# Kernel tuning notes

Hardware: AMD Instinct MI355X
Metric: run time of the kernel (lower is better)

## Reference

```python
import jax, jax.numpy as jnp
import numpy as np

N, E = 50000, 800000
IN, HID, OUT, H = 128, 16, 16, 4


def setup_inputs() -> dict:
    key = jax.random.key(0)
    ks = jax.random.split(key, 11)
    sc = 0.1
    return {
        "features": jax.random.normal(ks[0], (N, IN), jnp.float32),
        "src": jax.random.randint(ks[1], (E,), 0, N, dtype=jnp.int64) if jax.config.jax_enable_x64 else jax.random.randint(ks[1], (E,), 0, N).astype(jnp.int32),
        "dst": jax.random.randint(ks[2], (E,), 0, N).astype(jnp.int32),
        "W1": jax.random.normal(ks[3], (H * HID, IN), jnp.float32) * sc,
        "al1": jax.random.normal(ks[4], (H, HID), jnp.float32) * sc,
        "ar1": jax.random.normal(ks[5], (H, HID), jnp.float32) * sc,
        "b1": jax.random.normal(ks[6], (H * HID,), jnp.float32) * sc,
        "W2": jax.random.normal(ks[7], (H * OUT, H * HID), jnp.float32) * sc,
        "al2": jax.random.normal(ks[8], (H, OUT), jnp.float32) * sc,
        "ar2": jax.random.normal(ks[9], (H, OUT), jnp.float32) * sc,
        "b2": jax.random.normal(ks[10], (H * OUT,), jnp.float32) * sc,
    }


def gat_conv(src, dst, feat, W, al, ar, b, heads, dout):
    """DGL-style GATConv: fc -> edge attention -> dst-softmax -> scatter-sum."""
    n = feat.shape[0]
    h = (feat @ W.T).reshape(n, heads, dout)            # [N,H,D]
    el = jnp.einsum("nhd,hd->nh", h, al)                # [N,H]
    er = jnp.einsum("nhd,hd->nh", h, ar)                # [N,H]
    e = jax.nn.leaky_relu(el[src] + er[dst], 0.2)       # [E,H]
    m = jax.ops.segment_max(e, dst, num_segments=n)     # per-dst max, [N,H]
    a = jnp.exp(e - m[dst])                             # [E,H]
    s = jax.ops.segment_sum(a, dst, num_segments=n)     # [N,H]
    alpha = a / s[dst]                                  # edge softmax, [E,H]
    out = jax.ops.segment_sum(alpha[:, :, None] * h[src], dst, num_segments=n)
    return out + b.reshape(1, heads, dout)              # [N,H,D]


def reference(features, src, dst, W1, al1, ar1, b1, W2, al2, ar2, b2):
    h = gat_conv(src, dst, features, W1, al1, ar1, b1, H, HID).reshape(N, H * HID)
    h = jax.nn.relu(h)
    h = gat_conv(src, dst, h, W2, al2, ar2, b2, H, OUT).mean(axis=1)  # mean over heads
    return jax.nn.log_softmax(h, axis=1)
```

## Files before the change

### kernel.cpp

```cpp
#include <hip/hip_runtime.h>
#include <math.h>

#define N_NODES 50000
#define N_EDGES 800000
#define NPART 8
#define PART_SZ ((N_NODES + NPART - 1) / NPART)
#define CAP 64
#define SCAT_BLOCKS 2048

typedef __attribute__((ext_vector_type(8))) short short8;
typedef __attribute__((ext_vector_type(8))) unsigned short ushort8;
typedef __attribute__((ext_vector_type(4))) float v4f;
typedef __attribute__((ext_vector_type(2))) float v2f;
typedef __attribute__((ext_vector_type(4))) int int4v;

__device__ __forceinline__ float bf2f(unsigned short h) {
    return __uint_as_float(((unsigned int)h) << 16);
}
__device__ __forceinline__ unsigned short f2bf(float f) {
    unsigned int u = __float_as_uint(f);
    u += 0x7fff + ((u >> 16) & 1);
    return (unsigned short)(u >> 16);
}

__device__ __forceinline__ short8 load_afrag(const float* X, size_t row, int K,
                                             int kc, int quad) {
    const float* p = X + row * K + kc * 32 + quad * 8;
    const float4 t0 = *(const float4*)p;
    const float4 t1 = *(const float4*)(p + 4);
    short8 a;
    a[0] = (short)f2bf(t0.x); a[1] = (short)f2bf(t0.y);
    a[2] = (short)f2bf(t0.z); a[3] = (short)f2bf(t0.w);
    a[4] = (short)f2bf(t1.x); a[5] = (short)f2bf(t1.y);
    a[6] = (short)f2bf(t1.z); a[7] = (short)f2bf(t1.w);
    return a;
}
__device__ __forceinline__ short8 load_afrag(const unsigned short* X, size_t row,
                                             int K, int kc, int quad) {
    return *(const short8*)(X + row * K + kc * 32 + quad * 8);
}

template <int K, typename XT>
__global__ __launch_bounds__(256) void fc_att_mfma(
    const XT* __restrict__ X, const float* __restrict__ W,
    const float* __restrict__ al, const float* __restrict__ ar,
    unsigned short* __restrict__ Hout, float* __restrict__ el,
    float* __restrict__ er, int nTiles)
{
    constexpr int KP = K + 4;
    constexpr int NKC = K / 32;
    __shared__ float Wlds[64 * KP];
    const int tid = threadIdx.x;
    for (int i = tid; i < 64 * K; i += 256) {
        int r = i / K, c = i - r * K;
        Wlds[r * KP + c] = W[i];
    }
    __syncthreads();

    const int lane = tid & 63;
    const int wave = tid >> 6;
    const int d = lane & 15;
    const int quad = lane >> 4;

    short8 wf[4][NKC];
#pragma unroll
    for (int ng = 0; ng < 4; ++ng) {
#pragma unroll
        for (int kc = 0; kc < NKC; ++kc) {
            const float* wp = &Wlds[(ng * 16 + d) * KP + kc * 32 + quad * 8];
            const v4f w0 = *(const v4f*)wp;
            const v4f w1 = *(const v4f*)(wp + 4);
            short8 f;
            f[0] = (short)f2bf(w0[0]); f[1] = (short)f2bf(w0[1]);
            f[2] = (short)f2bf(w0[2]); f[3] = (short)f2bf(w0[3]);
            f[4] = (short)f2bf(w1[0]); f[5] = (short)f2bf(w1[1]);
            f[6] = (short)f2bf(w1[2]); f[7] = (short)f2bf(w1[3]);
            wf[ng][kc] = f;
        }
    }

    const int tile = blockIdx.x * 4 + wave;
    if (tile >= nTiles) return;
    const int node0 = tile * 16;

    v4f cc[4] = {{0.f,0.f,0.f,0.f},{0.f,0.f,0.f,0.f},{0.f,0.f,0.f,0.f},{0.f,0.f,0.f,0.f}};
#pragma unroll
    for (int kc = 0; kc < NKC; ++kc) {
        const short8 a = load_afrag(X, (size_t)(node0 + d), K, kc, quad);
        cc[0] = __builtin_amdgcn_mfma_f32_16x16x32_bf16(a, wf[0][kc], cc[0], 0, 0, 0);
        cc[1] = __builtin_amdgcn_mfma_f32_16x16x32_bf16(a, wf[1][kc], cc[1], 0, 0, 0);
        cc[2] = __builtin_amdgcn_mfma_f32_16x16x32_bf16(a, wf[2][kc], cc[2], 0, 0, 0);
        cc[3] = __builtin_amdgcn_mfma_f32_16x16x32_bf16(a, wf[3][kc], cc[3], 0, 0, 0);
    }

#pragma unroll
    for (int ng = 0; ng < 4; ++ng) {
        const float alv = al[ng * 16 + d];
        const float arv = ar[ng * 16 + d];
        const v4f c = cc[ng];
#pragma unroll
        for (int r = 0; r < 4; ++r) {
            const int node = node0 + quad * 4 + r;
            Hout[(size_t)node * 64 + ng * 16 + d] = f2bf(c[r]);
            float vel = c[r] * alv;
            float ver = c[r] * arv;
#pragma unroll
            for (int off = 1; off < 16; off <<= 1) {
                vel += __shfl_xor(vel, off);
                ver += __shfl_xor(ver, off);
            }
            if (d == 0) {
                el[node * 4 + ng] = vel;
                er[node * 4 + ng] = ver;
            }
        }
    }
}

__device__ __forceinline__ void scat1(int d, int s, int lo, int hi,
                                      int* __restrict__ cnt16,
                                      unsigned short* __restrict__ col)
{
    if (d >= lo && d < hi) {
        const int pos = atomicAdd(&cnt16[(unsigned)d * 16], 1);
        if (pos < CAP) col[(unsigned)d * CAP + pos] = (unsigned short)s;
    }
}

__global__ __launch_bounds__(256) void scatter_bucket_kernel(
    const int* __restrict__ src, const int* __restrict__ dst,
    int* __restrict__ cnt16, unsigned short* __restrict__ col)
{
    const int part = blockIdx.x & (NPART - 1);
    const int lo = part * PART_SZ;
    const int hi = lo + PART_SZ;
    const int tid_p = ((int)blockIdx.x >> 3) * 256 + threadIdx.x;
    const int stride = (SCAT_BLOCKS / NPART) * 256;
    const int4v* dst4 = (const int4v*)dst;
    const int4v* src4 = (const int4v*)src;
    const int NQ = N_EDGES / 4;
    for (int q = tid_p; q < NQ; q += 2 * stride) {
        const int q2 = q + stride;
        const bool ok2 = q2 < NQ;
        const int4v dA = __builtin_nontemporal_load(dst4 + q);
        const int4v sA = __builtin_nontemporal_load(src4 + q);
        const int4v dB = ok2 ? __builtin_nontemporal_load(dst4 + q2) : (int4v){-1,-1,-1,-1};
        const int4v sB = ok2 ? __builtin_nontemporal_load(src4 + q2) : (int4v){0,0,0,0};
        scat1(dA[0], sA[0], lo, hi, cnt16, col);
        scat1(dA[1], sA[1], lo, hi, cnt16, col);
        scat1(dA[2], sA[2], lo, hi, cnt16, col);
        scat1(dA[3], sA[3], lo, hi, cnt16, col);
        scat1(dB[0], sB[0], lo, hi, cnt16, col);
        scat1(dB[1], sB[1], lo, hi, cnt16, col);
        scat1(dB[2], sB[2], lo, hi, cnt16, col);
        scat1(dB[3], sB[3], lo, hi, cnt16, col);
    }
}

__device__ __forceinline__ void agg_walk_pair(
    const unsigned short* __restrict__ colrow, int len, int len_max,
    const float* __restrict__ el, const unsigned int* __restrict__ Hf32,
    int hb, int hl, float erv_a,
    float& accL_out, float& accH_out, float& sacc_a_out)
{
    const int j_a = hl >> 2;
    const unsigned h_a = (unsigned)(hl & 3);
    const int hd = hl >> 3;
    float accL0 = 0.f, accL1 = 0.f, accH0 = 0.f, accH1 = 0.f;
    float sacc_a = 0.f;
    for (int i = 0; i < len_max; i += 16) {
        const ushort8 sv0 = __builtin_nontemporal_load((const ushort8*)(colrow + i));
        const ushort8 sv1 = __builtin_nontemporal_load((const ushort8*)(colrow + i + 8));
        const int rm = len - i;
        const unsigned sa0 = (unsigned)colrow[i + j_a];
        const unsigned sa1 = (unsigned)colrow[i + 8 + j_a];
        float x0 = el[sa0 * 4u + h_a] + erv_a;
        float x1 = el[sa1 * 4u + h_a] + erv_a;
        x0 = fmaxf(x0, 0.2f * x0);
        x1 = fmaxf(x1, 0.2f * x1);
        float a0 = __expf(x0);
        float a1 = __expf(x1);
        a0 = (j_a < rm) ? a0 : 0.f;
        a1 = (j_a + 8 < rm) ? a1 : 0.f;
        sacc_a += a0 + a1;
        unsigned uu[16];
#pragma unroll
        for (int j = 0; j < 8; ++j)
            uu[j] = Hf32[(unsigned)sv0[j] * 32u + (unsigned)hl];
#pragma unroll
        for (int j = 0; j < 8; ++j)
            uu[8 + j] = Hf32[(unsigned)sv1[j] * 32u + (unsigned)hl];
#pragma unroll
        for (int j = 0; j < 8; ++j) {
            const float aj = __shfl(a0, hb + j * 4 + hd);
            const float lo = __uint_as_float(uu[j] << 16);
            const float hi = __uint_as_float(uu[j] & 0xffff0000u);
            if (j & 1) { accL1 = fmaf(aj, lo, accL1); accH1 = fmaf(aj, hi, accH1); }
            else       { accL0 = fmaf(aj, lo, accL0); accH0 = fmaf(aj, hi, accH0); }
        }
#pragma unroll
        for (int j = 0; j < 8; ++j) {
            const float aj = __shfl(a1, hb + j * 4 + hd);
            const float lo = __uint_as_float(uu[8 + j] << 16);
            const float hi = __uint_as_float(uu[8 + j] & 0xffff0000u);
            if (j & 1) { accL1 = fmaf(aj, lo, accL1); accH1 = fmaf(aj, hi, accH1); }
            else       { accL0 = fmaf(aj, lo, accL0); accH0 = fmaf(aj, hi, accH0); }
        }
    }
    sacc_a += __shfl_xor(sacc_a, 4);
    sacc_a += __shfl_xor(sacc_a, 8);
    sacc_a += __shfl_xor(sacc_a, 16);
    sacc_a_out = sacc_a;
    accL_out = accL0 + accL1;
    accH_out = accH0 + accH1;
}

__global__ __launch_bounds__(256) void agg_relu_kernel(
    const int* __restrict__ cnt16, const unsigned short* __restrict__ col,
    const float* __restrict__ el, const float* __restrict__ er,
    const unsigned int* __restrict__ Hf32, const float* __restrict__ b,
    unsigned int* __restrict__ out32, int n)
{
    const int lane = threadIdx.x & 63;
    const int wave = threadIdx.x >> 6;
    const int hl = lane & 31;
    const int hb = lane & 32;
    const int node = blockIdx.x * 8 + wave * 2 + (lane >> 5);
    if (node >= n) return;
    const int hd = hl >> 3;
    const int cg = hd * 16 + (hl & 7) * 2;
    const float erv_a = er[node * 4 + (hl & 3)];
    const int len = min(cnt16[(unsigned)node * 16], CAP);
    const int len_max = max(len, __shfl_xor(len, 32));
    float accL, accH, sacc_a;
    agg_walk_pair(col + (unsigned)node * CAP, len, len_max, el, Hf32,
                  hb, hl, erv_a, accL, accH, sacc_a);
    const float sc = __shfl(sacc_a, hb + hd);
    float vL = sc > 0.f ? accL / sc : 0.f;
    float vH = sc > 0.f ? accH / sc : 0.f;
    vL += b[cg];   vH += b[cg + 1];
    vL = vL > 0.f ? vL : 0.f;
    vH = vH > 0.f ? vH : 0.f;
    const unsigned u = (unsigned)f2bf(vL) | ((unsigned)f2bf(vH) << 16);
    __builtin_nontemporal_store(u, out32 + (size_t)node * 32 + hl);
}

__global__ __launch_bounds__(256) void agg_final_kernel(
    const int* __restrict__ cnt16, const unsigned short* __restrict__ col,
    const float* __restrict__ el, const float* __restrict__ er,
    const unsigned int* __restrict__ Hf32, const float* __restrict__ b,
    float* __restrict__ out, int n)
{
    const int lane = threadIdx.x & 63;
    const int wave = threadIdx.x >> 6;
    const int hl = lane & 31;
    const int hb = lane & 32;
    const int node = blockIdx.x * 8 + wave * 2 + (lane >> 5);
    if (node >= n) return;
    const int hd = hl >> 3;
    const int cg = hd * 16 + (hl & 7) * 2;
    const float erv_a = er[node * 4 + (hl & 3)];
    const int len = min(cnt16[(unsigned)node * 16], CAP);
    const int len_max = max(len, __shfl_xor(len, 32));
    float accL, accH, sacc_a;
    agg_walk_pair(col + (unsigned)node * CAP, len, len_max, el, Hf32,
                  hb, hl, erv_a, accL, accH, sacc_a);
    const float sc = __shfl(sacc_a, hb + hd);
    float zL = sc > 0.f ? accL / sc : 0.f;
    float zH = sc > 0.f ? accH / sc : 0.f;
    zL += b[cg];   zH += b[cg + 1];
    zL += __shfl_xor(zL, 8);  zL += __shfl_xor(zL, 16);  zL *= 0.25f;
    zH += __shfl_xor(zH, 8);  zH += __shfl_xor(zH, 16);  zH *= 0.25f;
    float m = fmaxf(zL, zH);
    m = fmaxf(m, __shfl_xor(m, 1));
    m = fmaxf(m, __shfl_xor(m, 2));
    m = fmaxf(m, __shfl_xor(m, 4));
    float se = __expf(zL - m) + __expf(zH - m);
    se += __shfl_xor(se, 1);
    se += __shfl_xor(se, 2);
    se += __shfl_xor(se, 4);
    const float lse = __logf(se);
    if (hl < 8) {
        v2f r;
        r[0] = zL - m - lse;
        r[1] = zH - m - lse;
        __builtin_nontemporal_store(r, (v2f*)(out + (size_t)node * 16 + hl * 2));
    }
}

extern "C" void kernel_launch(void* const* d_in, const int* in_sizes, int n_in,
                              void* d_out, int out_size, void* d_ws, size_t ws_size,
                              hipStream_t stream)
{
    const float* feat = (const float*)d_in[0];
    const int*   src  = (const int*)d_in[1];
    const int*   dst  = (const int*)d_in[2];
    const float* W1   = (const float*)d_in[3];
    const float* al1  = (const float*)d_in[4];
    const float* ar1  = (const float*)d_in[5];
    const float* b1   = (const float*)d_in[6];
    const float* W2   = (const float*)d_in[7];
    const float* al2  = (const float*)d_in[8];
    const float* ar2  = (const float*)d_in[9];
    const float* b2   = (const float*)d_in[10];
    float* out = (float*)d_out;

    float* el  = (float*)d_ws;
    float* er  = el + N_NODES * 4;
    int*   cnt16 = (int*)(er + N_NODES * 4);
    uintptr_t p = ((uintptr_t)(cnt16 + N_NODES * 16) + 15) & ~(uintptr_t)15;
    unsigned short* col = (unsigned short*)p;
    unsigned short* A   = col + (size_t)N_NODES * CAP + 64;
    unsigned short* B   = A + (size_t)N_NODES * 64;

    const int NT = N_NODES / 16;
    const int FB = (NT + 3) / 4;
    const int AB2 = (N_NODES + 7) / 8;

    (void)hipMemsetAsync(cnt16, 0, (size_t)((char*)A - (char*)cnt16), stream);
    scatter_bucket_kernel<<<SCAT_BLOCKS, 256, 0, stream>>>(src, dst, cnt16, col);

    fc_att_mfma<128, float><<<FB, 256, 0, stream>>>(feat, W1, al1, ar1, A, el, er, NT);
    agg_relu_kernel<<<AB2, 256, 0, stream>>>(cnt16, col, el, er,
                                             (const unsigned int*)A, b1,
                                             (unsigned int*)B, N_NODES);

    fc_att_mfma<64, unsigned short><<<FB, 256, 0, stream>>>(B, W2, al2, ar2, A, el, er, NT);
    agg_final_kernel<<<AB2, 256, 0, stream>>>(cnt16, col, el, er,
                                              (const unsigned int*)A, b2, out, N_NODES);
}
```

Baseline: 198.3 us.

## Fuse fc1 with edge scatter and layer-1 aggregation with fc2

The edge-bucketing scatter and the first dense projection now run in one launch, with block ranges assigned to each role, so the two independent stages overlap. Layer-1 aggregation now keeps each 16-node tile of ReLU'd hidden features in shared memory and feeds it straight into the fc2 MFMA. This removes the round trip of the intermediate matrix through global memory and cuts two kernel launches. Weights are now read from global memory directly instead of being staged in LDS. The fused aggregation runs one wave per 16 nodes, serially over 8 node pairs, which lowers parallelism in that stage compared with the earlier 8 nodes per block.

```diff
diff --git a/kernel.cpp b/kernel.cpp
--- a/kernel.cpp
+++ b/kernel.cpp
@@ -6,6 +6,7 @@
 #define NPART 8
 #define PART_SZ ((N_NODES + NPART - 1) / NPART)
 #define CAP 64
+#define FC1_BLOCKS 784
 #define SCAT_BLOCKS 2048
 
 typedef __attribute__((ext_vector_type(8))) short short8;
@@ -35,64 +36,49 @@
     a[6] = (short)f2bf(t1.z); a[7] = (short)f2bf(t1.w);
     return a;
 }
-__device__ __forceinline__ short8 load_afrag(const unsigned short* X, size_t row,
-                                             int K, int kc, int quad) {
-    return *(const short8*)(X + row * K + kc * 32 + quad * 8);
-}
-
-template <int K, typename XT>
-__global__ __launch_bounds__(256) void fc_att_mfma(
-    const XT* __restrict__ X, const float* __restrict__ W,
+
+template <int K>
+__device__ __forceinline__ void load_wfrags(const float* __restrict__ W,
+                                            int d, int quad, short8 wf[4][K / 32]) {
+#pragma unroll
+    for (int ng = 0; ng < 4; ++ng) {
+#pragma unroll
+        for (int kc = 0; kc < K / 32; ++kc) {
+            const float* wp = W + (size_t)(ng * 16 + d) * K + kc * 32 + quad * 8;
+            const float4 w0 = *(const float4*)wp;
+            const float4 w1 = *(const float4*)(wp + 4);
+            short8 f;
+            f[0] = (short)f2bf(w0.x); f[1] = (short)f2bf(w0.y);
+            f[2] = (short)f2bf(w0.z); f[3] = (short)f2bf(w0.w);
+            f[4] = (short)f2bf(w1.x); f[5] = (short)f2bf(w1.y);
+            f[6] = (short)f2bf(w1.z); f[7] = (short)f2bf(w1.w);
+            wf[ng][kc] = f;
+        }
+    }
+}
+
+template <int K>
+__device__ __forceinline__ void fc_body_nolds(
+    const float* __restrict__ X, const float* __restrict__ W,
     const float* __restrict__ al, const float* __restrict__ ar,
     unsigned short* __restrict__ Hout, float* __restrict__ el,
-    float* __restrict__ er, int nTiles)
-{
-    constexpr int KP = K + 4;
-    constexpr int NKC = K / 32;
-    __shared__ float Wlds[64 * KP];
-    const int tid = threadIdx.x;
-    for (int i = tid; i < 64 * K; i += 256) {
-        int r = i / K, c = i - r * K;
-        Wlds[r * KP + c] = W[i];
-    }
-    __syncthreads();
-
-    const int lane = tid & 63;
-    const int wave = tid >> 6;
+    float* __restrict__ er, int tile, int nTiles, int lane)
+{
+    if (tile >= nTiles) return;
     const int d = lane & 15;
     const int quad = lane >> 4;
-
-    short8 wf[4][NKC];
-#pragma unroll
-    for (int ng = 0; ng < 4; ++ng) {
-#pragma unroll
-        for (int kc = 0; kc < NKC; ++kc) {
-            const float* wp = &Wlds[(ng * 16 + d) * KP + kc * 32 + quad * 8];
-            const v4f w0 = *(const v4f*)wp;
-            const v4f w1 = *(const v4f*)(wp + 4);
-            short8 f;
-            f[0] = (short)f2bf(w0[0]); f[1] = (short)f2bf(w0[1]);
-            f[2] = (short)f2bf(w0[2]); f[3] = (short)f2bf(w0[3]);
-            f[4] = (short)f2bf(w1[0]); f[5] = (short)f2bf(w1[1]);
-            f[6] = (short)f2bf(w1[2]); f[7] = (short)f2bf(w1[3]);
-            wf[ng][kc] = f;
-        }
-    }
-
-    const int tile = blockIdx.x * 4 + wave;
-    if (tile >= nTiles) return;
+    short8 wf[4][K / 32];
+    load_wfrags<K>(W, d, quad, wf);
     const int node0 = tile * 16;
-
     v4f cc[4] = {{0.f,0.f,0.f,0.f},{0.f,0.f,0.f,0.f},{0.f,0.f,0.f,0.f},{0.f,0.f,0.f,0.f}};
 #pragma unroll
-    for (int kc = 0; kc < NKC; ++kc) {
+    for (int kc = 0; kc < K / 32; ++kc) {
         const short8 a = load_afrag(X, (size_t)(node0 + d), K, kc, quad);
         cc[0] = __builtin_amdgcn_mfma_f32_16x16x32_bf16(a, wf[0][kc], cc[0], 0, 0, 0);
         cc[1] = __builtin_amdgcn_mfma_f32_16x16x32_bf16(a, wf[1][kc], cc[1], 0, 0, 0);
         cc[2] = __builtin_amdgcn_mfma_f32_16x16x32_bf16(a, wf[2][kc], cc[2], 0, 0, 0);
         cc[3] = __builtin_amdgcn_mfma_f32_16x16x32_bf16(a, wf[3][kc], cc[3], 0, 0, 0);
     }
-
 #pragma unroll
     for (int ng = 0; ng < 4; ++ng) {
         const float alv = al[ng * 16 + d];
@@ -127,14 +113,14 @@
     }
 }
 
-__global__ __launch_bounds__(256) void scatter_bucket_kernel(
+__device__ __forceinline__ void scatter_body(
     const int* __restrict__ src, const int* __restrict__ dst,
-    int* __restrict__ cnt16, unsigned short* __restrict__ col)
-{
-    const int part = blockIdx.x & (NPART - 1);
+    int* __restrict__ cnt16, unsigned short* __restrict__ col,
+    int part, int sblk)
+{
     const int lo = part * PART_SZ;
     const int hi = lo + PART_SZ;
-    const int tid_p = ((int)blockIdx.x >> 3) * 256 + threadIdx.x;
+    const int tid_p = sblk * 256 + (int)threadIdx.x;
     const int stride = (SCAT_BLOCKS / NPART) * 256;
     const int4v* dst4 = (const int4v*)dst;
     const int4v* src4 = (const int4v*)src;
@@ -154,6 +140,25 @@
         scat1(dB[1], sB[1], lo, hi, cnt16, col);
         scat1(dB[2], sB[2], lo, hi, cnt16, col);
         scat1(dB[3], sB[3], lo, hi, cnt16, col);
+    }
+}
+
+__global__ __launch_bounds__(256) void fc1_scatter_fused(
+    const float* __restrict__ feat, const float* __restrict__ W1,
+    const float* __restrict__ al1, const float* __restrict__ ar1,
+    unsigned short* __restrict__ A, float* __restrict__ el1,
+    float* __restrict__ er1, int nTiles,
+    const int* __restrict__ src, const int* __restrict__ dst,
+    int* __restrict__ cnt16, unsigned short* __restrict__ col)
+{
+    if ((int)blockIdx.x < FC1_BLOCKS) {
+        const int tile = blockIdx.x * 4 + (threadIdx.x >> 6);
+        fc_body_nolds<128>(feat, W1, al1, ar1, A, el1, er1, tile, nTiles,
+                           threadIdx.x & 63);
+    } else {
+        const int part = blockIdx.x & (NPART - 1);
+        const int sblk = ((int)blockIdx.x - FC1_BLOCKS) >> 3;
+        scatter_body(src, dst, cnt16, col, part, sblk);
     }
 }
 
@@ -215,34 +220,83 @@
     accH_out = accH0 + accH1;
 }
 
-__global__ __launch_bounds__(256) void agg_relu_kernel(
+__global__ __launch_bounds__(256) void agg_fc2_fused(
     const int* __restrict__ cnt16, const unsigned short* __restrict__ col,
-    const float* __restrict__ el, const float* __restrict__ er,
-    const unsigned int* __restrict__ Hf32, const float* __restrict__ b,
-    unsigned int* __restrict__ out32, int n)
-{
+    const float* __restrict__ el1, const float* __restrict__ er1,
+    const unsigned int* __restrict__ A32, const float* __restrict__ b1,
+    const float* __restrict__ W2, const float* __restrict__ al2,
+    const float* __restrict__ ar2, unsigned short* __restrict__ C,
+    float* __restrict__ el2, float* __restrict__ er2, int nTiles)
+{
+    __shared__ unsigned short hs[4][16][72];
     const int lane = threadIdx.x & 63;
     const int wave = threadIdx.x >> 6;
+    const int tile = blockIdx.x * 4 + wave;
+    const bool valid = tile < nTiles;
     const int hl = lane & 31;
     const int hb = lane & 32;
-    const int node = blockIdx.x * 8 + wave * 2 + (lane >> 5);
-    if (node >= n) return;
     const int hd = hl >> 3;
     const int cg = hd * 16 + (hl & 7) * 2;
-    const float erv_a = er[node * 4 + (hl & 3)];
-    const int len = min(cnt16[(unsigned)node * 16], CAP);
-    const int len_max = max(len, __shfl_xor(len, 32));
-    float accL, accH, sacc_a;
-    agg_walk_pair(col + (unsigned)node * CAP, len, len_max, el, Hf32,
-                  hb, hl, erv_a, accL, accH, sacc_a);
-    const float sc = __shfl(sacc_a, hb + hd);
-    float vL = sc > 0.f ? accL / sc : 0.f;
-    float vH = sc > 0.f ? accH / sc : 0.f;
-    vL += b[cg];   vH += b[cg + 1];
-    vL = vL > 0.f ? vL : 0.f;
-    vH = vH > 0.f ? vH : 0.f;
-    const unsigned u = (unsigned)f2bf(vL) | ((unsigned)f2bf(vH) << 16);
-    __builtin_nontemporal_store(u, out32 + (size_t)node * 32 + hl);
+
+    if (valid) {
+#pragma unroll 1
+        for (int r = 0; r < 8; ++r) {
+            const int node = tile * 16 + 2 * r + (lane >> 5);
+            const float erv_a = el1 == er1 ? 0.f : er1[node * 4 + (hl & 3)];
+            const int len = min(cnt16[(unsigned)node * 16], CAP);
+            const int len_max = max(len, __shfl_xor(len, 32));
+            float accL, accH, sacc_a;
+            agg_walk_pair(col + (unsigned)node * CAP, len, len_max, el1, A32,
+                          hb, hl, erv_a, accL, accH, sacc_a);
+            const float sc = __shfl(sacc_a, hb + hd);
+            float vL = sc > 0.f ? accL / sc : 0.f;
+            float vH = sc > 0.f ? accH / sc : 0.f;
+            vL += b1[cg];   vH += b1[cg + 1];
+            vL = fmaxf(vL, 0.f);
+            vH = fmaxf(vH, 0.f);
+            const unsigned u = (unsigned)f2bf(vL) | ((unsigned)f2bf(vH) << 16);
+            *(unsigned int*)&hs[wave][2 * r + (lane >> 5)][cg] = u;
+        }
+    }
+    __syncthreads();
+    if (valid) {
+        const int d = lane & 15;
+        const int quad = lane >> 4;
+        short8 wf[4][2];
+        load_wfrags<64>(W2, d, quad, wf);
+        v4f cc[4] = {{0.f,0.f,0.f,0.f},{0.f,0.f,0.f,0.f},{0.f,0.f,0.f,0.f},{0.f,0.f,0.f,0.f}};
+#pragma unroll
+        for (int kc = 0; kc < 2; ++kc) {
+            const short8 a = *(const short8*)&hs[wave][d][kc * 32 + quad * 8];
+            cc[0] = __builtin_amdgcn_mfma_f32_16x16x32_bf16(a, wf[0][kc], cc[0], 0, 0, 0);
+            cc[1] = __builtin_amdgcn_mfma_f32_16x16x32_bf16(a, wf[1][kc], cc[1], 0, 0, 0);
+            cc[2] = __builtin_amdgcn_mfma_f32_16x16x32_bf16(a, wf[2][kc], cc[2], 0, 0, 0);
+            cc[3] = __builtin_amdgcn_mfma_f32_16x16x32_bf16(a, wf[3][kc], cc[3], 0, 0, 0);
+        }
+        const int node0 = tile * 16;
+#pragma unroll
+        for (int ng = 0; ng < 4; ++ng) {
+            const float alv = al2[ng * 16 + d];
+            const float arv = ar2[ng * 16 + d];
+            const v4f c = cc[ng];
+#pragma unroll
+            for (int r = 0; r < 4; ++r) {
+                const int node = node0 + quad * 4 + r;
+                C[(size_t)node * 64 + ng * 16 + d] = f2bf(c[r]);
+                float vel = c[r] * alv;
+                float ver = c[r] * arv;
+#pragma unroll
+                for (int off = 1; off < 16; off <<= 1) {
+                    vel += __shfl_xor(vel, off);
+                    ver += __shfl_xor(ver, off);
+                }
+                if (d == 0) {
+                    el2[node * 4 + ng] = vel;
+                    er2[node * 4 + ng] = ver;
+                }
+            }
+        }
+    }
 }
 
 __global__ __launch_bounds__(256) void agg_final_kernel(
@@ -305,27 +359,29 @@
     const float* b2   = (const float*)d_in[10];
     float* out = (float*)d_out;
 
-    float* el  = (float*)d_ws;
-    float* er  = el + N_NODES * 4;
-    int*   cnt16 = (int*)(er + N_NODES * 4);
+    float* el1 = (float*)d_ws;
+    float* er1 = el1 + N_NODES * 4;
+    float* el2 = er1 + N_NODES * 4;
+    float* er2 = el2 + N_NODES * 4;
+    int*   cnt16 = (int*)(er2 + N_NODES * 4);
     uintptr_t p = ((uintptr_t)(cnt16 + N_NODES * 16) + 15) & ~(uintptr_t)15;
     unsigned short* col = (unsigned short*)p;
     unsigned short* A   = col + (size_t)N_NODES * CAP + 64;
-    unsigned short* B   = A + (size_t)N_NODES * 64;
+    unsigned short* C   = A + (size_t)N_NODES * 64;
 
     const int NT = N_NODES / 16;
     const int FB = (NT + 3) / 4;
     const int AB2 = (N_NODES + 7) / 8;
 
     (void)hipMemsetAsync(cnt16, 0, (size_t)((char*)A - (char*)cnt16), stream);
-    scatter_bucket_kernel<<<SCAT_BLOCKS, 256, 0, stream>>>(src, dst, cnt16, col);
-
-    fc_att_mfma<128, float><<<FB, 256, 0, stream>>>(feat, W1, al1, ar1, A, el, er, NT);
-    agg_relu_kernel<<<AB2, 256, 0, stream>>>(cnt16, col, el, er,
-                                             (const unsigned int*)A, b1,
-                                             (unsigned int*)B, N_NODES);
-
-    fc_att_mfma<64, unsigned short><<<FB, 256, 0, stream>>>(B, W2, al2, ar2, A, el, er, NT);
-    agg_final_kernel<<<AB2, 256, 0, stream>>>(cnt16, col, el, er,
-                                              (const unsigned int*)A, b2, out, N_NODES);
-}
+
+    fc1_scatter_fused<<<FC1_BLOCKS + SCAT_BLOCKS, 256, 0, stream>>>(
+        feat, W1, al1, ar1, A, el1, er1, NT, src, dst, cnt16, col);
+
+    agg_fc2_fused<<<FB, 256, 0, stream>>>(cnt16, col, el1, er1,
+                                          (const unsigned int*)A, b1,
+                                          W2, al2, ar2, C, el2, er2, NT);
+
+    agg_final_kernel<<<AB2, 256, 0, stream>>>(cnt16, col, el2, er2,
+                                              (const unsigned int*)C, b2, out, N_NODES);
+}
```

Result: no change. 200.1 us (+0.9%).
